# Performance work log

Hardware: AMD Instinct MI355X
Metric: run time of the kernel (lower is better)

## Reference

```python
import jax, jax.numpy as jnp
import numpy as np

N, D, P, K = 200000, 256, 65536, 8
TEMP = 0.2


def _l2norm(x, eps=1e-12):
    # matches torch F.normalize(p=2): divide by clamped L2 norm
    n = jnp.sqrt(jnp.sum(x * x, axis=-1, keepdims=True))
    return x / jnp.maximum(n, eps)


def setup_inputs() -> dict:
    key = jax.random.key(0)
    ks = jax.random.split(key, 8)
    node_emb = jax.random.normal(ks[0], (N, D), jnp.float32)
    # xavier-ish scale for the bias-free projection weights
    W_src = jax.random.normal(ks[1], (D, D), jnp.float32) / np.float32(np.sqrt(D))
    W_dst = jax.random.normal(ks[2], (D, D), jnp.float32) / np.float32(np.sqrt(D))
    pos_src = jax.random.randint(ks[3], (P,), 0, N)
    pos_dst = jax.random.randint(ks[4], (P,), 0, N)
    pos_sign = jax.random.randint(ks[5], (P,), 0, 3)  # {0: negative-sign edge, 1: positive, 2: masked}
    neg_src = jax.random.randint(ks[6], (P * K,), 0, N)
    neg_dst = jax.random.randint(ks[7], (P * K,), 0, N)
    return {"node_emb": node_emb, "W_src": W_src, "W_dst": W_dst,
            "pos_src": pos_src, "pos_dst": pos_dst, "pos_sign": pos_sign,
            "neg_src": neg_src, "neg_dst": neg_dst}


def reference(node_emb, W_src, W_dst, pos_src, pos_dst, pos_sign, neg_src, neg_dst):
    z = _l2norm(node_emb)                                   # [N, D]
    # nn.Linear(x) = x @ W.T (no bias)
    u = _l2norm(z[pos_src] @ W_src.T)                       # [P, D]
    v = _l2norm(z[pos_dst] @ W_dst.T)                       # [P, D]
    sim_pos = jnp.sum(u * v, axis=-1)                       # [P]
    mult = jnp.where(pos_sign == 0, -1.0, 1.0).astype(sim_pos.dtype)
    sim_pos = sim_pos * mult
    use_mask = (pos_sign != 2).astype(sim_pos.dtype)        # [P]
    u_neg = _l2norm(z[neg_src] @ W_src.T)                   # [P*K, D]
    v_neg = _l2norm(z[neg_dst] @ W_dst.T)                   # [P*K, D]
    sim_neg = jnp.sum(u_neg * v_neg, axis=-1).reshape(P, K) # [P, K]
    logits = jnp.concatenate([sim_pos[:, None], sim_neg], axis=1) / TEMP  # [P, 1+K]
    # cross-entropy with label 0 for every row
    loss_all = jax.nn.logsumexp(logits, axis=-1) - logits[:, 0]           # [P]
    return jnp.sum(loss_all * use_mask) / (jnp.sum(use_mask) + 1e-9)
```

## Files before the change

### kernel.cpp

```cpp
#include <hip/hip_runtime.h>
#include <hip/hip_bf16.h>
#include <cstdint>
#include <cstddef>

#define N_NODES 200000
#define DIM 256
#define P_EDGES 65536
#define INV_TEMP 5.0f
#define NBLK_EDGE (P_EDGES / 16)

typedef __attribute__((ext_vector_type(8))) short short8;
typedef __attribute__((ext_vector_type(4))) float f32x4;

__device__ __forceinline__ unsigned short f2bf(float f) {
    unsigned int x = __float_as_uint(f);
    x = (x + 0x7FFFu + ((x >> 16) & 1u)) >> 16;
    return (unsigned short)x;
}
__device__ __forceinline__ float bf2f(unsigned short u) {
    return __uint_as_float(((unsigned int)u) << 16);
}

__global__ void convert_w(const float* __restrict__ Wsrc, const float* __restrict__ Wdst,
                          unsigned short* __restrict__ Wsb, unsigned short* __restrict__ Wdb) {
    int g = blockIdx.x * blockDim.x + threadIdx.x;
    const float4* src;
    unsigned short* dst;
    int off;
    if (g < 16384) { src = (const float4*)Wsrc; dst = Wsb; off = g; }
    else           { src = (const float4*)Wdst; dst = Wdb; off = g - 16384; }
    float4 v = src[off];
    ushort4 h;
    h.x = f2bf(v.x); h.y = f2bf(v.y); h.z = f2bf(v.z); h.w = f2bf(v.w);
    *reinterpret_cast<ushort4*>(dst + (size_t)off * 4) = h;
}

__global__ __launch_bounds__(512) void proj_gemm(
    const float* __restrict__ emb,
    const unsigned short* __restrict__ Wsb,
    const unsigned short* __restrict__ Wdb,
    unsigned short* __restrict__ Zs,
    unsigned short* __restrict__ Zd)
{
    __shared__ unsigned short As[64][264];
    __shared__ float partial[8][64];
    const int row0 = blockIdx.x * 64;

    {
        const float4* e4 = (const float4*)(emb + (size_t)row0 * DIM);
        const int t = threadIdx.x;
        #pragma unroll
        for (int i = 0; i < 8; ++i) {
            const int g = i * 512 + t;
            float4 v = e4[g];
            ushort4 h;
            h.x = f2bf(v.x); h.y = f2bf(v.y); h.z = f2bf(v.z); h.w = f2bf(v.w);
            *reinterpret_cast<ushort4*>(&As[g >> 6][(g & 63) * 4]) = h;
        }
    }
    __syncthreads();

    const int lane = threadIdx.x & 63;
    const int wv = threadIdx.x >> 6;
    const int mat = wv >> 2;
    const int cq = wv & 3;
    const int l15 = lane & 15;
    const int grp = lane >> 4;

    const unsigned short* __restrict__ W = mat ? Wdb : Wsb;
    unsigned short* __restrict__ out = mat ? Zd : Zs;

    f32x4 acc[4][4];
    #pragma unroll
    for (int nt = 0; nt < 4; ++nt)
        #pragma unroll
        for (int ft = 0; ft < 4; ++ft) acc[nt][ft] = (f32x4){0.f, 0.f, 0.f, 0.f};

    #pragma unroll
    for (int ks = 0; ks < 8; ++ks) {
        const int k0 = ks * 32 + grp * 8;
        short8 ef[4], wf[4];
        #pragma unroll
        for (int nt = 0; nt < 4; ++nt)
            ef[nt] = *reinterpret_cast<const short8*>(&As[nt * 16 + l15][k0]);
        #pragma unroll
        for (int ft = 0; ft < 4; ++ft)
            wf[ft] = *reinterpret_cast<const short8*>(
                W + (size_t)(cq * 64 + ft * 16 + l15) * DIM + k0);
        #pragma unroll
        for (int nt = 0; nt < 4; ++nt)
            #pragma unroll
            for (int ft = 0; ft < 4; ++ft)
                acc[nt][ft] = __builtin_amdgcn_mfma_f32_16x16x32_bf16(
                    wf[ft], ef[nt], acc[nt][ft], 0, 0, 0);
    }

    #pragma unroll
    for (int nt = 0; nt < 4; ++nt) {
        float ssq = 0.f;
        #pragma unroll
        for (int ft = 0; ft < 4; ++ft)
            #pragma unroll
            for (int r = 0; r < 4; ++r) { float x = acc[nt][ft][r]; ssq += x * x; }
        ssq += __shfl_xor(ssq, 16);
        ssq += __shfl_xor(ssq, 32);
        if (grp == 0) partial[wv][nt * 16 + l15] = ssq;
    }
    __syncthreads();

    #pragma unroll
    for (int nt = 0; nt < 4; ++nt) {
        const int node = nt * 16 + l15;
        const float tot = partial[mat * 4 + 0][node] + partial[mat * 4 + 1][node]
                        + partial[mat * 4 + 2][node] + partial[mat * 4 + 3][node];
        const float inv = rsqrtf(fmaxf(tot, 1e-24f));
        unsigned short* orow = out + (size_t)(row0 + node) * DIM + cq * 64 + grp * 4;
        #pragma unroll
        for (int ft = 0; ft < 4; ++ft) {
            ushort4 h;
            h.x = f2bf(acc[nt][ft][0] * inv);
            h.y = f2bf(acc[nt][ft][1] * inv);
            h.z = f2bf(acc[nt][ft][2] * inv);
            h.w = f2bf(acc[nt][ft][3] * inv);
            *reinterpret_cast<ushort4*>(orow + ft * 16) = h;
        }
    }
}

__global__ __launch_bounds__(256) void edge_loss(
    const unsigned short* __restrict__ Zs,
    const unsigned short* __restrict__ Zd,
    const int* __restrict__ pos_src, const int* __restrict__ pos_dst,
    const int* __restrict__ pos_sign,
    const int* __restrict__ neg_src, const int* __restrict__ neg_dst,
    float* __restrict__ partials)
{
    const int tid = threadIdx.x;
    const int l15 = tid & 15;
    const int g = tid >> 4;
    const int p = blockIdx.x * 16 + g;

    int su[9], sv[9];
    su[0] = pos_src[p]; sv[0] = pos_dst[p];
    #pragma unroll
    for (int k = 0; k < 8; ++k) { su[k + 1] = neg_src[p * 8 + k]; sv[k + 1] = neg_dst[p * 8 + k]; }

    float sims[9];
    #pragma unroll
    for (int j = 0; j < 9; ++j) {
        const unsigned short* ur = Zs + (size_t)su[j] * DIM + l15 * 16;
        const unsigned short* vr = Zd + (size_t)sv[j] * DIM + l15 * 16;
        short8 u0 = *reinterpret_cast<const short8*>(ur);
        short8 u1 = *reinterpret_cast<const short8*>(ur + 8);
        short8 v0 = *reinterpret_cast<const short8*>(vr);
        short8 v1 = *reinterpret_cast<const short8*>(vr + 8);
        float s = 0.f;
        #pragma unroll
        for (int i = 0; i < 8; ++i) {
            s += bf2f((unsigned short)u0[i]) * bf2f((unsigned short)v0[i]);
            s += bf2f((unsigned short)u1[i]) * bf2f((unsigned short)v1[i]);
        }
        s += __shfl_xor(s, 1);
        s += __shfl_xor(s, 2);
        s += __shfl_xor(s, 4);
        s += __shfl_xor(s, 8);
        sims[j] = s;
    }

    const int sg = pos_sign[p];
    float ln[9];
    ln[0] = (sg == 0 ? -sims[0] : sims[0]) * INV_TEMP;
    float m = ln[0];
    #pragma unroll
    for (int j = 1; j < 9; ++j) { ln[j] = sims[j] * INV_TEMP; m = fmaxf(m, ln[j]); }
    float se = 0.f;
    #pragma unroll
    for (int j = 0; j < 9; ++j) se += __expf(ln[j] - m);
    const float loss = m + __logf(se) - ln[0];
    const float use = (sg != 2) ? 1.f : 0.f;

    __shared__ float wl[16], wc[16];
    if (l15 == 0) { wl[g] = loss * use; wc[g] = use; }
    __syncthreads();
    if (tid == 0) {
        float L = 0.f, C = 0.f;
        #pragma unroll
        for (int i = 0; i < 16; ++i) { L += wl[i]; C += wc[i]; }
        partials[blockIdx.x * 2 + 0] = L;
        partials[blockIdx.x * 2 + 1] = C;
    }
}

__global__ __launch_bounds__(256) void finalize(const float* __restrict__ partials,
                                                float* __restrict__ out) {
    const int tid = threadIdx.x;
    float L = 0.f, C = 0.f;
    for (int i = tid; i < NBLK_EDGE; i += 256) {
        L += partials[i * 2 + 0];
        C += partials[i * 2 + 1];
    }
    #pragma unroll
    for (int s = 32; s >= 1; s >>= 1) {
        L += __shfl_xor(L, s);
        C += __shfl_xor(C, s);
    }
    __shared__ float sl[4], sc[4];
    if ((tid & 63) == 0) { sl[tid >> 6] = L; sc[tid >> 6] = C; }
    __syncthreads();
    if (tid == 0) {
        float Lt = sl[0] + sl[1] + sl[2] + sl[3];
        float Ct = sc[0] + sc[1] + sc[2] + sc[3];
        out[0] = Lt / (Ct + 1e-9f);
    }
}

extern "C" void kernel_launch(void* const* d_in, const int* in_sizes, int n_in,
                              void* d_out, int out_size, void* d_ws, size_t ws_size,
                              hipStream_t stream) {
    const float* node_emb = (const float*)d_in[0];
    const float* W_src    = (const float*)d_in[1];
    const float* W_dst    = (const float*)d_in[2];
    const int* pos_src    = (const int*)d_in[3];
    const int* pos_dst    = (const int*)d_in[4];
    const int* pos_sign   = (const int*)d_in[5];
    const int* neg_src    = (const int*)d_in[6];
    const int* neg_dst    = (const int*)d_in[7];
    float* out = (float*)d_out;

    char* ws = (char*)d_ws;
    const size_t zbytes = (size_t)N_NODES * DIM * 2;
    unsigned short* Zs  = (unsigned short*)ws;
    unsigned short* Zd  = (unsigned short*)(ws + zbytes);
    unsigned short* Wsb = (unsigned short*)(ws + 2 * zbytes);
    unsigned short* Wdb = Wsb + DIM * DIM;
    float* partials = (float*)(Wdb + DIM * DIM);

    hipLaunchKernelGGL(convert_w, dim3(128), dim3(256), 0, stream,
                       W_src, W_dst, Wsb, Wdb);
    hipLaunchKernelGGL(proj_gemm, dim3(N_NODES / 64), dim3(512), 0, stream,
                       node_emb, Wsb, Wdb, Zs, Zd);
    hipLaunchKernelGGL(edge_loss, dim3(NBLK_EDGE), dim3(256), 0, stream,
                       Zs, Zd, pos_src, pos_dst, pos_sign, neg_src, neg_dst, partials);
    hipLaunchKernelGGL(finalize, dim3(1), dim3(256), 0, stream, partials, out);
}
```

Before: 527.3 us.

## Pre-convert embeddings to bf16 and use persistent double-buffered async-LDS GEMM

Adds a separate pass that converts the full node embedding table to bf16 in workspace. The projection GEMM becomes persistent (512 blocks of 256 threads) and prefetches the next 64-row tile into a second LDS buffer with global_load_lds, using an XOR-swizzled layout. Each wave now computes 128 output columns instead of 64. The intent is to overlap tile loads with MFMA work and avoid bank conflicts, at the cost of an extra full write and re-read of the bf16 embedding table (~100MB of extra traffic).

```diff
diff --git a/kernel.cpp b/kernel.cpp
--- a/kernel.cpp
+++ b/kernel.cpp
@@ -8,6 +8,8 @@
 #define P_EDGES 65536
 #define INV_TEMP 5.0f
 #define NBLK_EDGE (P_EDGES / 16)
+#define NTILES (N_NODES / 64)
+#define GEMM_BLOCKS 512
 
 typedef __attribute__((ext_vector_type(8))) short short8;
 typedef __attribute__((ext_vector_type(4))) float f32x4;
@@ -21,109 +23,137 @@
     return __uint_as_float(((unsigned int)u) << 16);
 }
 
-__global__ void convert_w(const float* __restrict__ Wsrc, const float* __restrict__ Wdst,
-                          unsigned short* __restrict__ Wsb, unsigned short* __restrict__ Wdb) {
-    int g = blockIdx.x * blockDim.x + threadIdx.x;
-    const float4* src;
-    unsigned short* dst;
-    int off;
-    if (g < 16384) { src = (const float4*)Wsrc; dst = Wsb; off = g; }
-    else           { src = (const float4*)Wdst; dst = Wdb; off = g - 16384; }
-    float4 v = src[off];
-    ushort4 h;
-    h.x = f2bf(v.x); h.y = f2bf(v.y); h.z = f2bf(v.z); h.w = f2bf(v.w);
-    *reinterpret_cast<ushort4*>(dst + (size_t)off * 4) = h;
-}
-
-__global__ __launch_bounds__(512) void proj_gemm(
-    const float* __restrict__ emb,
+__device__ __forceinline__ void gload_lds16(const unsigned short* g, unsigned short* l) {
+    __builtin_amdgcn_global_load_lds(
+        (const __attribute__((address_space(1))) unsigned int*)(g),
+        (__attribute__((address_space(3))) unsigned int*)(l),
+        16, 0, 0);
+}
+
+__global__ __launch_bounds__(256) void convert_all(
+    const float* __restrict__ emb, const float* __restrict__ Wsrc,
+    const float* __restrict__ Wdst,
+    unsigned short* __restrict__ embB, unsigned short* __restrict__ Wsb,
+    unsigned short* __restrict__ Wdb)
+{
+    const long stride = (long)gridDim.x * 256;
+    const long total_emb = (long)N_NODES * DIM / 4;
+    for (long i = (long)blockIdx.x * 256 + threadIdx.x; i < total_emb; i += stride) {
+        float4 v = ((const float4*)emb)[i];
+        ushort4 h;
+        h.x = f2bf(v.x); h.y = f2bf(v.y); h.z = f2bf(v.z); h.w = f2bf(v.w);
+        ((ushort4*)embB)[i] = h;
+    }
+    for (long i = (long)blockIdx.x * 256 + threadIdx.x; i < 2 * DIM * DIM / 4; i += stride) {
+        const float4* src = (i < DIM * DIM / 4) ? (const float4*)Wsrc : (const float4*)Wdst;
+        unsigned short* dst = (i < DIM * DIM / 4) ? Wsb : Wdb;
+        long off = i & (DIM * DIM / 4 - 1);
+        float4 v = src[off];
+        ushort4 h;
+        h.x = f2bf(v.x); h.y = f2bf(v.y); h.z = f2bf(v.z); h.w = f2bf(v.w);
+        *reinterpret_cast<ushort4*>(dst + off * 4) = h;
+    }
+}
+
+__global__ __launch_bounds__(256, 2) void proj_gemm(
+    const unsigned short* __restrict__ embB,
     const unsigned short* __restrict__ Wsb,
     const unsigned short* __restrict__ Wdb,
     unsigned short* __restrict__ Zs,
     unsigned short* __restrict__ Zd)
 {
-    __shared__ unsigned short As[64][264];
-    __shared__ float partial[8][64];
-    const int row0 = blockIdx.x * 64;
-
-    {
-        const float4* e4 = (const float4*)(emb + (size_t)row0 * DIM);
-        const int t = threadIdx.x;
-        #pragma unroll
-        for (int i = 0; i < 8; ++i) {
-            const int g = i * 512 + t;
-            float4 v = e4[g];
-            ushort4 h;
-            h.x = f2bf(v.x); h.y = f2bf(v.y); h.z = f2bf(v.z); h.w = f2bf(v.w);
-            *reinterpret_cast<ushort4*>(&As[g >> 6][(g & 63) * 4]) = h;
-        }
-    }
-    __syncthreads();
-
-    const int lane = threadIdx.x & 63;
-    const int wv = threadIdx.x >> 6;
-    const int mat = wv >> 2;
-    const int cq = wv & 3;
+    __shared__ unsigned short As[2][64 * 256];
+    __shared__ float partial[4][64];
+
+    const int tid = threadIdx.x;
+    const int lane = tid & 63;
+    const int wv = tid >> 6;
     const int l15 = lane & 15;
     const int grp = lane >> 4;
-
-    const unsigned short* __restrict__ W = mat ? Wdb : Wsb;
+    const int mat = wv >> 1;
+    const int half = wv & 1;
+    const int e3 = l15 & 7;
+
+    const unsigned short* __restrict__ W = (mat ? Wdb : Wsb) + (size_t)(half * 128) * DIM;
     unsigned short* __restrict__ out = mat ? Zd : Zs;
 
-    f32x4 acc[4][4];
-    #pragma unroll
-    for (int nt = 0; nt < 4; ++nt)
-        #pragma unroll
-        for (int ft = 0; ft < 4; ++ft) acc[nt][ft] = (f32x4){0.f, 0.f, 0.f, 0.f};
-
-    #pragma unroll
-    for (int ks = 0; ks < 8; ++ks) {
-        const int k0 = ks * 32 + grp * 8;
-        short8 ef[4], wf[4];
+    auto STAGE = [&](int t, int b) {
+        const unsigned short* gt = embB + (size_t)t * (64 * 256);
+        #pragma unroll
+        for (int i = 0; i < 8; ++i) {
+            const int s = wv * 512 + i * 64 + lane;
+            const int r = s >> 5;
+            const int cd = (s & 31) ^ (r & 7);
+            gload_lds16(gt + r * 256 + cd * 8, &As[b][(wv * 512 + i * 64) * 8]);
+        }
+    };
+
+    int t = blockIdx.x;
+    int cur = 0;
+    STAGE(t, 0);
+    __syncthreads();
+
+    for (; t < NTILES; t += GEMM_BLOCKS) {
+        const int tn = t + GEMM_BLOCKS;
+        if (tn < NTILES) STAGE(tn, cur ^ 1);
+
+        f32x4 acc[4][8];
         #pragma unroll
         for (int nt = 0; nt < 4; ++nt)
-            ef[nt] = *reinterpret_cast<const short8*>(&As[nt * 16 + l15][k0]);
-        #pragma unroll
-        for (int ft = 0; ft < 4; ++ft)
-            wf[ft] = *reinterpret_cast<const short8*>(
-                W + (size_t)(cq * 64 + ft * 16 + l15) * DIM + k0);
-        #pragma unroll
-        for (int nt = 0; nt < 4; ++nt)
-            #pragma unroll
-            for (int ft = 0; ft < 4; ++ft)
-                acc[nt][ft] = __builtin_amdgcn_mfma_f32_16x16x32_bf16(
-                    wf[ft], ef[nt], acc[nt][ft], 0, 0, 0);
-    }
-
-    #pragma unroll
-    for (int nt = 0; nt < 4; ++nt) {
-        float ssq = 0.f;
-        #pragma unroll
-        for (int ft = 0; ft < 4; ++ft)
-            #pragma unroll
-            for (int r = 0; r < 4; ++r) { float x = acc[nt][ft][r]; ssq += x * x; }
-        ssq += __shfl_xor(ssq, 16);
-        ssq += __shfl_xor(ssq, 32);
-        if (grp == 0) partial[wv][nt * 16 + l15] = ssq;
-    }
-    __syncthreads();
-
-    #pragma unroll
-    for (int nt = 0; nt < 4; ++nt) {
-        const int node = nt * 16 + l15;
-        const float tot = partial[mat * 4 + 0][node] + partial[mat * 4 + 1][node]
-                        + partial[mat * 4 + 2][node] + partial[mat * 4 + 3][node];
-        const float inv = rsqrtf(fmaxf(tot, 1e-24f));
-        unsigned short* orow = out + (size_t)(row0 + node) * DIM + cq * 64 + grp * 4;
-        #pragma unroll
-        for (int ft = 0; ft < 4; ++ft) {
-            ushort4 h;
-            h.x = f2bf(acc[nt][ft][0] * inv);
-            h.y = f2bf(acc[nt][ft][1] * inv);
-            h.z = f2bf(acc[nt][ft][2] * inv);
-            h.w = f2bf(acc[nt][ft][3] * inv);
-            *reinterpret_cast<ushort4*>(orow + ft * 16) = h;
-        }
+            #pragma unroll
+            for (int f = 0; f < 8; ++f) acc[nt][f] = (f32x4){0.f, 0.f, 0.f, 0.f};
+
+        #pragma unroll
+        for (int ks = 0; ks < 8; ++ks) {
+            const int c = ((ks << 2) | grp) ^ e3;
+            short8 ef[4];
+            #pragma unroll
+            for (int nt = 0; nt < 4; ++nt)
+                ef[nt] = *reinterpret_cast<const short8*>(
+                    &As[cur][(nt * 16 + l15) * 256 + c * 8]);
+            #pragma unroll
+            for (int f = 0; f < 8; ++f) {
+                short8 wf = *reinterpret_cast<const short8*>(
+                    W + (size_t)(f * 16 + l15) * DIM + ks * 32 + grp * 8);
+                #pragma unroll
+                for (int nt = 0; nt < 4; ++nt)
+                    acc[nt][f] = __builtin_amdgcn_mfma_f32_16x16x32_bf16(
+                        wf, ef[nt], acc[nt][f], 0, 0, 0);
+            }
+        }
+
+        #pragma unroll
+        for (int nt = 0; nt < 4; ++nt) {
+            float ssq = 0.f;
+            #pragma unroll
+            for (int f = 0; f < 8; ++f)
+                #pragma unroll
+                for (int r = 0; r < 4; ++r) { float x = acc[nt][f][r]; ssq += x * x; }
+            ssq += __shfl_xor(ssq, 16);
+            ssq += __shfl_xor(ssq, 32);
+            if (grp == 0) partial[wv][nt * 16 + l15] = ssq;
+        }
+        __syncthreads();
+
+        const int row0 = t * 64;
+        #pragma unroll
+        for (int nt = 0; nt < 4; ++nt) {
+            const int node = nt * 16 + l15;
+            const float tot = partial[mat * 2 + 0][node] + partial[mat * 2 + 1][node];
+            const float inv = rsqrtf(fmaxf(tot, 1e-24f));
+            unsigned short* orow = out + (size_t)(row0 + node) * DIM + half * 128 + grp * 4;
+            #pragma unroll
+            for (int f = 0; f < 8; ++f) {
+                ushort4 h;
+                h.x = f2bf(acc[nt][f][0] * inv);
+                h.y = f2bf(acc[nt][f][1] * inv);
+                h.z = f2bf(acc[nt][f][2] * inv);
+                h.w = f2bf(acc[nt][f][3] * inv);
+                *reinterpret_cast<ushort4*>(orow + f * 16) = h;
+            }
+        }
+        __syncthreads();
+        cur ^= 1;
     }
 }
 
@@ -208,9 +238,8 @@
     if ((tid & 63) == 0) { sl[tid >> 6] = L; sc[tid >> 6] = C; }
     __syncthreads();
     if (tid == 0) {
-        float Lt = sl[0] + sl[1] + sl[2] + sl[3];
-        float Ct = sc[0] + sc[1] + sc[2] + sc[3];
-        out[0] = Lt / (Ct + 1e-9f);
+        out[0] = (sl[0] + sl[1] + sl[2] + sl[3]) /
+                 (sc[0] + sc[1] + sc[2] + sc[3] + 1e-9f);
     }
 }
 
@@ -229,16 +258,17 @@
 
     char* ws = (char*)d_ws;
     const size_t zbytes = (size_t)N_NODES * DIM * 2;
-    unsigned short* Zs  = (unsigned short*)ws;
-    unsigned short* Zd  = (unsigned short*)(ws + zbytes);
-    unsigned short* Wsb = (unsigned short*)(ws + 2 * zbytes);
-    unsigned short* Wdb = Wsb + DIM * DIM;
+    unsigned short* embB = (unsigned short*)ws;
+    unsigned short* Zs   = (unsigned short*)(ws + zbytes);
+    unsigned short* Zd   = (unsigned short*)(ws + 2 * zbytes);
+    unsigned short* Wsb  = (unsigned short*)(ws + 3 * zbytes);
+    unsigned short* Wdb  = Wsb + DIM * DIM;
     float* partials = (float*)(Wdb + DIM * DIM);
 
-    hipLaunchKernelGGL(convert_w, dim3(128), dim3(256), 0, stream,
-                       W_src, W_dst, Wsb, Wdb);
-    hipLaunchKernelGGL(proj_gemm, dim3(N_NODES / 64), dim3(512), 0, stream,
-                       node_emb, Wsb, Wdb, Zs, Zd);
+    hipLaunchKernelGGL(convert_all, dim3(2048), dim3(256), 0, stream,
+                       node_emb, W_src, W_dst, embB, Wsb, Wdb);
+    hipLaunchKernelGGL(proj_gemm, dim3(GEMM_BLOCKS), dim3(256), 0, stream,
+                       embB, Wsb, Wdb, Zs, Zd);
     hipLaunchKernelGGL(edge_loss, dim3(NBLK_EDGE), dim3(256), 0, stream,
                        Zs, Zd, pos_src, pos_dst, pos_sign, neg_src, neg_dst, partials);
     hipLaunchKernelGGL(finalize, dim3(1), dim3(256), 0, stream, partials, out);
```

Result: slower. 612.3 us (+16.1%).
